# Kernel optimization log

Measured on AMD Instinct MI355X. Metric: run time of the kernel, lower is better.

The kernel has to match this reference:

```python
import jax, jax.numpy as jnp
import numpy as np

N = 50000          # nodes
E = 500000         # edges
EMB = 64           # hidden_size
R = 2              # DDE num_rounds
RR = 2             # DDE num_reverse_rounds
PRED_IN = 4 * EMB + 4 + 4 * (R + RR)  # 276


def setup_inputs() -> dict:
    key = jax.random.key(0)
    ks = jax.random.split(key, 10)
    x = jax.random.normal(ks[0], (N, EMB), jnp.float32)
    edge_index = jax.random.randint(ks[1], (2, E), 0, N, dtype=jnp.int64)
    edge_attr = jax.random.normal(ks[2], (E, EMB), jnp.float32)
    topic_signal = jax.random.uniform(ks[3], (N, 2), dtype=jnp.float32)
    q_emb = jax.random.normal(ks[4], (E, EMB), jnp.float32)
    # learned parameters
    non_text_emb = jax.random.normal(ks[5], (1, EMB), jnp.float32)
    W1 = jax.random.normal(ks[6], (PRED_IN, EMB), jnp.float32) / np.sqrt(PRED_IN)
    b1 = jnp.zeros((EMB,), jnp.float32)
    W2 = jax.random.normal(ks[7], (EMB, 1), jnp.float32) / np.sqrt(EMB)
    b2 = jnp.zeros((1,), jnp.float32)
    return dict(x=x, edge_index=edge_index, edge_attr=edge_attr,
                topic_signal=topic_signal, q_emb=q_emb,
                non_text_emb=non_text_emb, W1=W1, b1=b1, W2=W2, b2=b2)


def _segment_mean(data, seg, num_segments):
    # mean aggregation as in PyG MessagePassing(aggr='mean'); empty segments -> 0
    s = jax.ops.segment_sum(data, seg, num_segments=num_segments)
    cnt = jax.ops.segment_sum(jnp.ones((seg.shape[0],), data.dtype), seg,
                              num_segments=num_segments)
    return s / jnp.maximum(cnt, 1.0)[:, None]


def reference(x, edge_index, edge_attr, topic_signal, q_emb,
              non_text_emb, W1, b1, W2, b2):
    src, dst = edge_index[0], edge_index[1]
    # replace all-zero node rows with the learned non-text entity embedding
    zero_mask = jnp.all(x == 0, axis=1)
    x = jnp.where(zero_mask[:, None], non_text_emb[0], x)

    feats = [x, topic_signal]  # topic_pe = True
    # DDE forward rounds: aggregate src -> dst along edge_index
    h = topic_signal
    for _ in range(R):
        h = _segment_mean(h[src], dst, N)
        feats.append(h)
    # DDE reverse rounds: flipped edges (dst -> src)
    h = topic_signal
    for _ in range(RR):
        h = _segment_mean(h[dst], src, N)
        feats.append(h)

    h_e = jnp.concatenate(feats, axis=1)                      # [N, EMB+2+2*(R+RR)]
    h_triple = jnp.concatenate([q_emb, h_e[src], edge_attr, h_e[dst]], axis=1)  # [E, PRED_IN]
    hidden = jax.nn.relu(h_triple @ W1 + b1)                  # [E, EMB]
    return (hidden @ W2 + b2).squeeze(-1)                     # [E]
```

## Files before the change

### kernel.cpp

```cpp
#include <hip/hip_runtime.h>
#include <cstdint>
#include <cstddef>


typedef __bf16 bf16x8 __attribute__((ext_vector_type(8)));
typedef float f32x4 __attribute__((ext_vector_type(4)));

__device__ __forceinline__ unsigned int f2bf1(float f) {
    unsigned int u = __float_as_uint(f);
    return (u + 0x7fffu + ((u >> 16) & 1u)) >> 16;
}
__device__ __forceinline__ unsigned int pk2(float a, float b) {
    return f2bf1(a) | (f2bf1(b) << 16);
}
__device__ __forceinline__ bf16x8 cvt8v(float4 a, float4 b) {
    bf16x8 r;
    r[0] = (__bf16)a.x; r[1] = (__bf16)a.y; r[2] = (__bf16)a.z; r[3] = (__bf16)a.w;
    r[4] = (__bf16)b.x; r[5] = (__bf16)b.y; r[6] = (__bf16)b.z; r[7] = (__bf16)b.w;
    return r;
}

#define GL16(gp, lp)                                                        \
    __builtin_amdgcn_global_load_lds(                                       \
        (const __attribute__((address_space(1))) void*)(gp),                \
        (__attribute__((address_space(3))) void*)(lp), 16, 0, 0)


__global__ void k_detect(const int* __restrict__ idx, int E, int* __restrict__ flag) {
    int e = blockIdx.x * blockDim.x + threadIdx.x;
    bool nz = (e < E) && (idx[2 * e + 1] != 0);
    unsigned long long m = __ballot(nz);
    if (m != 0ull && (threadIdx.x & 63) == 0) atomicOr(flag, 1);
}

__global__ void k_convert(const int* __restrict__ idx, int E, const int* __restrict__ flag,
                          int* __restrict__ src_i, int* __restrict__ dst_i,
                          int* __restrict__ cnt_dst, int* __restrict__ cnt_src,
                          unsigned short* __restrict__ pos_f, unsigned short* __restrict__ pos_r) {
    int e = blockIdx.x * blockDim.x + threadIdx.x;
    if (e >= E) return;
    int s, d;
    if (*flag) { s = idx[e];     d = idx[E + e]; }
    else       { s = idx[2 * e]; d = idx[2 * E + 2 * e]; }
    src_i[e] = s; dst_i[e] = d;
    pos_f[e] = (unsigned short)atomicAdd(&cnt_dst[d], 1);
    pos_r[e] = (unsigned short)atomicAdd(&cnt_src[s], 1);
}

__global__ void k_scan(const int* __restrict__ cnt_dst, const int* __restrict__ cnt_src,
                       int* __restrict__ off_f, int* __restrict__ off_r, int N) {
    const int* cnt = (blockIdx.x == 0) ? cnt_dst : cnt_src;
    int* off       = (blockIdx.x == 0) ? off_f   : off_r;
    const int t = threadIdx.x;
    const int C = (N + 1023) / 1024;
    int lo = t * C, hi = lo + C; if (hi > N) hi = N; if (lo > N) lo = N;
    int sum = 0;
    for (int i = lo; i < hi; ++i) sum += cnt[i];
    __shared__ int wsum[16];
    int lane = t & 63, wv = t >> 6;
    int v = sum;
    for (int ofs = 1; ofs < 64; ofs <<= 1) {
        int u = __shfl_up(v, ofs);
        if (lane >= ofs) v += u;
    }
    if (lane == 63) wsum[wv] = v;
    __syncthreads();
    if (wv == 0) {
        int x = (lane < 16) ? wsum[lane] : 0;
        for (int ofs = 1; ofs < 16; ofs <<= 1) {
            int u = __shfl_up(x, ofs);
            if (lane >= ofs) x += u;
        }
        if (lane < 16) wsum[lane] = x;
    }
    __syncthreads();
    int base = (wv > 0 ? wsum[wv - 1] : 0) + (v - sum);
    for (int i = lo; i < hi; ++i) { off[i] = base; base += cnt[i]; }
}

__global__ void k_fill(const int* __restrict__ src_i, const int* __restrict__ dst_i,
                       const unsigned short* __restrict__ pos_f, const unsigned short* __restrict__ pos_r,
                       const int* __restrict__ off_f, const int* __restrict__ off_r,
                       int* __restrict__ csr_f, int* __restrict__ csr_r, int E) {
    int e = blockIdx.x * blockDim.x + threadIdx.x;
    if (e >= E) return;
    int s = src_i[e], d = dst_i[e];
    csr_f[off_f[d] + pos_f[e]] = s;
    csr_r[off_r[s] + pos_r[e]] = d;
}

__global__ void k_round(const int* __restrict__ off_f, const int* __restrict__ csr_f,
                        const int* __restrict__ off_r, const int* __restrict__ csr_r,
                        const float* __restrict__ hf_in,
                        const float* __restrict__ hr_in,
                        float* __restrict__ f_out, float* __restrict__ r_out,
                        int N, int E) {
    int gid = blockIdx.x * blockDim.x + threadIdx.x;
    if (gid >= 2 * N) return;
    const bool rev = gid >= N;
    const int n = rev ? gid - N : gid;
    const int* __restrict__ off = rev ? off_r : off_f;
    const int* __restrict__ csr = rev ? csr_r : csr_f;
    const float2* __restrict__ h = (const float2*)(rev ? hr_in : hf_in);
    float2* __restrict__ o = (float2*)(rev ? r_out : f_out);
    int b = off[n], e = (n + 1 < N) ? off[n + 1] : E;
    float sx = 0.f, sy = 0.f;
    for (int j = b; j < e; ++j) { float2 t = h[csr[j]]; sx += t.x; sy += t.y; }
    float inv = 1.0f / (float)max(e - b, 1);
    o[n] = make_float2(sx * inv, sy * inv);
}

__global__ void k_build(const float* __restrict__ x, const float* __restrict__ topic,
                        const float* __restrict__ nte,
                        const float* __restrict__ f1, const float* __restrict__ f2,
                        const float* __restrict__ r1, const float* __restrict__ r2,
                        unsigned short* __restrict__ he, int N) {
    int n = blockIdx.x * blockDim.x + threadIdx.x;
    if (n >= N) return;
    const float4* xr = (const float4*)(x + (size_t)n * 64);
    float4 v[16];
    bool allz = true;
#pragma unroll
    for (int i = 0; i < 16; ++i) {
        v[i] = xr[i];
        allz = allz && (v[i].x == 0.f && v[i].y == 0.f && v[i].z == 0.f && v[i].w == 0.f);
    }
    const float4* nr = (const float4*)nte;
    unsigned int row[40];
#pragma unroll
    for (int i = 0; i < 16; ++i) {
        float4 s = allz ? nr[i] : v[i];
        row[2 * i]     = pk2(s.x, s.y);
        row[2 * i + 1] = pk2(s.z, s.w);
    }
    row[32] = pk2(topic[2 * n], topic[2 * n + 1]);
    row[33] = pk2(f1[2 * n], f1[2 * n + 1]);
    row[34] = pk2(f2[2 * n], f2[2 * n + 1]);
    row[35] = pk2(r1[2 * n], r1[2 * n + 1]);
    row[36] = pk2(r2[2 * n], r2[2 * n + 1]);
    row[37] = 0u; row[38] = 0u; row[39] = 0u;
    uint4* dst = (uint4*)(he + (size_t)n * 80);
#pragma unroll
    for (int i = 0; i < 10; ++i) dst[i] = ((const uint4*)row)[i];
}

__global__ void k_w1t(const float* __restrict__ W1, unsigned short* __restrict__ W1T) {
    int i = blockIdx.x * blockDim.x + threadIdx.x;
    if (i >= 64 * 288) return;
    int col = i / 288, pk = i - col * 288;
    int k = 0; bool valid = true;
    if (pk < 64)       { k = pk; }
    else if (pk < 128) { k = 138 + (pk - 64); }
    else if (pk < 208) { int j = pk - 128; k = 64 + j;  valid = j < 74; }
    else               { int j = pk - 208; k = 202 + j; valid = j < 74; }
    float v = valid ? W1[k * 64 + col] : 0.f;
    W1T[col * 288 + pk] = (unsigned short)f2bf1(v);
}


__launch_bounds__(128, 2)
__global__ void k_gemm(const float* __restrict__ q_emb,
                       const float* __restrict__ edge_attr,
                       const unsigned short* __restrict__ he,
                       const unsigned short* __restrict__ W1Tg,
                       const int* __restrict__ src_i, const int* __restrict__ dst_i,
                       const float* __restrict__ b1, const float* __restrict__ W2,
                       const float* __restrict__ b2, float* __restrict__ out, int E)
{
    __shared__ __align__(64) char smem[57344];
    const int tid = threadIdx.x;
    const int w = tid >> 6, l = tid & 63, c = l & 15, q = l >> 4;
    const int NW = gridDim.x * 2;
    const int gw = blockIdx.x * 2 + w;
    const int ntiles = E / 16;

#pragma unroll
    for (int jj = 0; jj < 18; ++jj) {
        int j = w * 18 + jj;
        GL16((const char*)W1Tg + j * 1024 + l * 16, smem + j * 1024);
    }

    char* buf0 = smem + 36864 + (w * 2) * 5120;
    char* buf1 = buf0 + 5120;

    int T = gw;
    {
        int e0 = T * 16 + (l & 15);
        int s0 = src_i[e0], d0 = dst_i[e0];
#pragma unroll
        for (int j = 0; j < 5; ++j) {
            int ch = j * 4 + (l >> 4);
            int node = ch < 10 ? s0 : d0;
            int chunk = ch < 10 ? ch : ch - 10;
            GL16((const char*)he + (size_t)node * 160 + chunk * 16, buf0 + j * 1024);
        }
    }
    const float* qr0 = q_emb     + (size_t)(T * 16 + c) * 64 + q * 8;
    const float* ar0 = edge_attr + (size_t)(T * 16 + c) * 64 + q * 8;
    float4 qc0 = *(const float4*)qr0,        qc1 = *(const float4*)(qr0 + 4);
    float4 qc2 = *(const float4*)(qr0 + 32), qc3 = *(const float4*)(qr0 + 36);
    float4 ec0 = *(const float4*)ar0,        ec1 = *(const float4*)(ar0 + 4);
    float4 ec2 = *(const float4*)(ar0 + 32), ec3 = *(const float4*)(ar0 + 36);
    int si_n, di_n;
    {
        int en = min(T + NW, ntiles - 1) * 16 + (l & 15);
        si_n = src_i[en]; di_n = dst_i[en];
    }
    float b1v[4], w2v[4];
#pragma unroll
    for (int ct = 0; ct < 4; ++ct) { b1v[ct] = b1[ct * 16 + c]; w2v[ct] = W2[ct * 16 + c]; }
    const float bb = b2[0];
    __syncthreads();

    int cur = 0;
    while (T < ntiles) {
        const int Tn = T + NW;
        const bool more = Tn < ntiles;
        float4 qn0, qn1, qn2, qn3, en0, en1, en2, en3;
        int si_f = si_n, di_f = di_n;
        char* sbuf = cur ? buf0 : buf1;
        char* cbuf = cur ? buf1 : buf0;

        if (more) {
            const float* qr = q_emb     + (size_t)(Tn * 16 + c) * 64 + q * 8;
            const float* ar = edge_attr + (size_t)(Tn * 16 + c) * 64 + q * 8;
            qn0 = *(const float4*)qr;        qn1 = *(const float4*)(qr + 4);
            qn2 = *(const float4*)(qr + 32); qn3 = *(const float4*)(qr + 36);
            en0 = *(const float4*)ar;        en1 = *(const float4*)(ar + 4);
            en2 = *(const float4*)(ar + 32); en3 = *(const float4*)(ar + 36);
#pragma unroll
            for (int j = 0; j < 5; ++j) {
                int ch = j * 4 + (l >> 4);
                int node = ch < 10 ? si_n : di_n;
                int chunk = ch < 10 ? ch : ch - 10;
                GL16((const char*)he + (size_t)node * 160 + chunk * 16, sbuf + j * 1024);
            }
            int ef = min(Tn + NW, ntiles - 1) * 16 + (l & 15);
            si_f = src_i[ef]; di_f = dst_i[ef];
            asm volatile("s_waitcnt vmcnt(15)" ::: "memory");
        } else {
            qn0 = qc0; qn1 = qc1; qn2 = qc2; qn3 = qc3;
            en0 = ec0; en1 = ec1; en2 = ec2; en3 = ec3;
            asm volatile("s_waitcnt vmcnt(0)" ::: "memory");
        }
        __builtin_amdgcn_sched_barrier(0);

        f32x4 acc0 = {}, acc1 = {}, acc2 = {}, acc3 = {};
        const char* wrow = smem + c * 576 + q * 16;
#define BF(ct, ks) (*(const bf16x8*)(wrow + (ct) * 9216 + (ks) * 64))
#define HEF(pl) (*(const bf16x8*)(cbuf + (pl) * 256 + c * 16))
#define KST(ks, A)                                                                 \
        {                                                                          \
            bf16x8 a_ = (A);                                                       \
            acc0 = __builtin_amdgcn_mfma_f32_16x16x32_bf16(a_, BF(0, ks), acc0, 0, 0, 0); \
            acc1 = __builtin_amdgcn_mfma_f32_16x16x32_bf16(a_, BF(1, ks), acc1, 0, 0, 0); \
            acc2 = __builtin_amdgcn_mfma_f32_16x16x32_bf16(a_, BF(2, ks), acc2, 0, 0, 0); \
            acc3 = __builtin_amdgcn_mfma_f32_16x16x32_bf16(a_, BF(3, ks), acc3, 0, 0, 0); \
        }
        KST(0, cvt8v(qc0, qc1))
        KST(1, cvt8v(qc2, qc3))
        KST(2, cvt8v(ec0, ec1))
        KST(3, cvt8v(ec2, ec3))
        KST(4, HEF(q))
        KST(5, HEF(q + 4))
        KST(6, HEF(q + 8))
        KST(7, HEF(q + 12))
        KST(8, HEF(q + 16))
#undef KST
#undef HEF
#undef BF

        float pr[4];
#pragma unroll
        for (int r = 0; r < 4; ++r) {
            float h0 = fmaxf(acc0[r] + b1v[0], 0.f);
            float h1 = fmaxf(acc1[r] + b1v[1], 0.f);
            float h2 = fmaxf(acc2[r] + b1v[2], 0.f);
            float h3 = fmaxf(acc3[r] + b1v[3], 0.f);
            float p = fmaf(h0, w2v[0], fmaf(h1, w2v[1], fmaf(h2, w2v[2], h3 * w2v[3])));
            p += __shfl_xor(p, 1);
            p += __shfl_xor(p, 2);
            p += __shfl_xor(p, 4);
            p += __shfl_xor(p, 8);
            pr[r] = p;
        }
        if (c == 0) {
            *(float4*)&out[T * 16 + q * 4] =
                make_float4(pr[0] + bb, pr[1] + bb, pr[2] + bb, pr[3] + bb);
        }

        qc0 = qn0; qc1 = qn1; qc2 = qn2; qc3 = qn3;
        ec0 = en0; ec1 = en1; ec2 = en2; ec3 = en3;
        si_n = si_f; di_n = di_f;
        T = Tn; cur ^= 1;
    }
}


extern "C" void kernel_launch(void* const* d_in, const int* in_sizes, int n_in,
                              void* d_out, int out_size, void* d_ws, size_t ws_size,
                              hipStream_t stream)
{
    const float* x         = (const float*)d_in[0];
    const int*   eidx      = (const int*)  d_in[1];
    const float* edge_attr = (const float*)d_in[2];
    const float* topic     = (const float*)d_in[3];
    const float* q_emb     = (const float*)d_in[4];
    const float* nte       = (const float*)d_in[5];
    const float* W1        = (const float*)d_in[6];
    const float* b1        = (const float*)d_in[7];
    const float* W2        = (const float*)d_in[8];
    const float* b2        = (const float*)d_in[9];
    float* out = (float*)d_out;

    const int E = out_size;
    const int N = in_sizes[0] / 64;

    char* ws = (char*)d_ws;
    int* flag  = (int*)ws;
    int* src_i = (int*)(ws + 16);
    int* dst_i = src_i + E;
    int* off_f = dst_i + E;
    int* off_r = off_f + N;
    float* fblk = (float*)(off_r + N);
    float* f1 = fblk;
    float* f2 = fblk + 2 * (size_t)N;
    float* r1 = fblk + 4 * (size_t)N;
    float* r2 = fblk + 6 * (size_t)N;
    int* cnt_dst = (int*)f1;
    int* cnt_src = cnt_dst + N;
    char* heblk = (char*)(fblk + 8 * (size_t)N);
    unsigned short* pos_f = (unsigned short*)heblk;
    unsigned short* pos_r = pos_f + E;
    int* csr_f = (int*)(pos_r + E);
    int* csr_r = csr_f + E;
    unsigned short* he = (unsigned short*)heblk;
    size_t he_bytes = (size_t)N * 160;
    size_t trans_bytes = (size_t)E * 12;
    size_t heblk_bytes = he_bytes > trans_bytes ? he_bytes : trans_bytes;
    unsigned short* W1T = (unsigned short*)(heblk + heblk_bytes);

    size_t needed = 16 + (size_t)8 * E + (size_t)8 * N + (size_t)32 * N + heblk_bytes + 64 * 288 * 2;
    if (ws_size < needed) return;

    hipMemsetAsync(flag, 0, 16, stream);
    hipMemsetAsync(cnt_dst, 0, (size_t)8 * N, stream);

    const int gE = (E + 255) / 256;
    const int gN = (N + 255) / 256;
    const int gN2 = (2 * N + 255) / 256;

    k_detect <<<gE, 256, 0, stream>>>(eidx, E, flag);
    k_convert<<<gE, 256, 0, stream>>>(eidx, E, flag, src_i, dst_i,
                                      cnt_dst, cnt_src, pos_f, pos_r);
    k_scan   <<<2, 1024, 0, stream>>>(cnt_dst, cnt_src, off_f, off_r, N);
    k_fill   <<<gE, 256, 0, stream>>>(src_i, dst_i, pos_f, pos_r, off_f, off_r,
                                      csr_f, csr_r, E);
    k_round  <<<gN2, 256, 0, stream>>>(off_f, csr_f, off_r, csr_r, topic, topic, f1, r1, N, E);
    k_round  <<<gN2, 256, 0, stream>>>(off_f, csr_f, off_r, csr_r, f1, r1, f2, r2, N, E);
    k_build  <<<gN, 256, 0, stream>>>(x, topic, nte, f1, f2, r1, r2, he, N);
    k_w1t    <<<(64 * 288 + 255) / 256, 256, 0, stream>>>(W1, W1T);

    k_gemm<<<512, 128, 0, stream>>>(q_emb, edge_attr, he, W1T,
                                    src_i, dst_i, b1, W2, b2, out, E);
}
```

Measured before the change: 559.1 us.

## Use fragment-ordered W1T layout, 4 waves per block, deeper index prefetch

Reorders the transposed bf16 W1 into MFMA fragment order so each lane's B-operand LDS read is contiguous (l*16 stride), which should remove bank conflicts from the old 576-byte row stride. Raises the GEMM block to 4 waves sharing one LDS copy of the weights, halving the weight staging per wave and doubling waves per CU. It also prefetches src/dst indices two tiles ahead to hide gather-address latency. The cost is larger LDS per block (77.8KB), which may limit blocks per CU, and more register pressure.

```diff
diff --git a/kernel.cpp b/kernel.cpp
--- a/kernel.cpp
+++ b/kernel.cpp
@@ -147,18 +147,23 @@
 __global__ void k_w1t(const float* __restrict__ W1, unsigned short* __restrict__ W1T) {
     int i = blockIdx.x * blockDim.x + threadIdx.x;
     if (i >= 64 * 288) return;
-    int col = i / 288, pk = i - col * 288;
+    int j = i & 7;
+    int l = (i >> 3) & 63;
+    int t36 = i >> 9;
+    int ks = t36 % 9, ct = t36 / 9;
+    int col = ct * 16 + (l & 15);
+    int pk = ks * 32 + (l >> 4) * 8 + j;
     int k = 0; bool valid = true;
     if (pk < 64)       { k = pk; }
     else if (pk < 128) { k = 138 + (pk - 64); }
-    else if (pk < 208) { int j = pk - 128; k = 64 + j;  valid = j < 74; }
-    else               { int j = pk - 208; k = 202 + j; valid = j < 74; }
+    else if (pk < 208) { int jj = pk - 128; k = 64 + jj;  valid = jj < 74; }
+    else               { int jj = pk - 208; k = 202 + jj; valid = jj < 74; }
     float v = valid ? W1[k * 64 + col] : 0.f;
-    W1T[col * 288 + pk] = (unsigned short)f2bf1(v);
-}
-
-
-__launch_bounds__(128, 2)
+    W1T[i] = (unsigned short)f2bf1(v);
+}
+
+
+__launch_bounds__(256, 2)
 __global__ void k_gemm(const float* __restrict__ q_emb,
                        const float* __restrict__ edge_attr,
                        const unsigned short* __restrict__ he,
@@ -167,29 +172,29 @@
                        const float* __restrict__ b1, const float* __restrict__ W2,
                        const float* __restrict__ b2, float* __restrict__ out, int E)
 {
-    __shared__ __align__(64) char smem[57344];
+    __shared__ __align__(64) char smem[77824];
     const int tid = threadIdx.x;
     const int w = tid >> 6, l = tid & 63, c = l & 15, q = l >> 4;
-    const int NW = gridDim.x * 2;
-    const int gw = blockIdx.x * 2 + w;
+    const int NW = gridDim.x * 4;
+    const int gw = blockIdx.x * 4 + w;
     const int ntiles = E / 16;
 
 #pragma unroll
-    for (int jj = 0; jj < 18; ++jj) {
-        int j = w * 18 + jj;
+    for (int jj = 0; jj < 9; ++jj) {
+        int j = w * 9 + jj;
         GL16((const char*)W1Tg + j * 1024 + l * 16, smem + j * 1024);
     }
 
-    char* buf0 = smem + 36864 + (w * 2) * 5120;
+    char* buf0 = smem + 36864 + w * 10240;
     char* buf1 = buf0 + 5120;
 
     int T = gw;
     {
-        int e0 = T * 16 + (l & 15);
+        int e0 = T * 16 + c;
         int s0 = src_i[e0], d0 = dst_i[e0];
 #pragma unroll
         for (int j = 0; j < 5; ++j) {
-            int ch = j * 4 + (l >> 4);
+            int ch = j * 4 + q;
             int node = ch < 10 ? s0 : d0;
             int chunk = ch < 10 ? ch : ch - 10;
             GL16((const char*)he + (size_t)node * 160 + chunk * 16, buf0 + j * 1024);
@@ -201,10 +206,12 @@
     float4 qc2 = *(const float4*)(qr0 + 32), qc3 = *(const float4*)(qr0 + 36);
     float4 ec0 = *(const float4*)ar0,        ec1 = *(const float4*)(ar0 + 4);
     float4 ec2 = *(const float4*)(ar0 + 32), ec3 = *(const float4*)(ar0 + 36);
-    int si_n, di_n;
+    int siA, diA, siB, diB;
     {
-        int en = min(T + NW, ntiles - 1) * 16 + (l & 15);
-        si_n = src_i[en]; di_n = dst_i[en];
+        int eA = min(T + NW, ntiles - 1) * 16 + c;
+        int eB = min(T + 2 * NW, ntiles - 1) * 16 + c;
+        siA = src_i[eA]; diA = dst_i[eA];
+        siB = src_i[eB]; diB = dst_i[eB];
     }
     float b1v[4], w2v[4];
 #pragma unroll
@@ -217,7 +224,7 @@
         const int Tn = T + NW;
         const bool more = Tn < ntiles;
         float4 qn0, qn1, qn2, qn3, en0, en1, en2, en3;
-        int si_f = si_n, di_f = di_n;
+        int siC = siB, diC = diB;
         char* sbuf = cur ? buf0 : buf1;
         char* cbuf = cur ? buf1 : buf0;
 
@@ -230,13 +237,13 @@
             en2 = *(const float4*)(ar + 32); en3 = *(const float4*)(ar + 36);
 #pragma unroll
             for (int j = 0; j < 5; ++j) {
-                int ch = j * 4 + (l >> 4);
-                int node = ch < 10 ? si_n : di_n;
+                int ch = j * 4 + q;
+                int node = ch < 10 ? siA : diA;
                 int chunk = ch < 10 ? ch : ch - 10;
                 GL16((const char*)he + (size_t)node * 160 + chunk * 16, sbuf + j * 1024);
             }
-            int ef = min(Tn + NW, ntiles - 1) * 16 + (l & 15);
-            si_f = src_i[ef]; di_f = dst_i[ef];
+            int eC = min(T + 3 * NW, ntiles - 1) * 16 + c;
+            siC = src_i[eC]; diC = dst_i[eC];
             asm volatile("s_waitcnt vmcnt(15)" ::: "memory");
         } else {
             qn0 = qc0; qn1 = qc1; qn2 = qc2; qn3 = qc3;
@@ -246,8 +253,8 @@
         __builtin_amdgcn_sched_barrier(0);
 
         f32x4 acc0 = {}, acc1 = {}, acc2 = {}, acc3 = {};
-        const char* wrow = smem + c * 576 + q * 16;
-#define BF(ct, ks) (*(const bf16x8*)(wrow + (ct) * 9216 + (ks) * 64))
+        const char* wbase = smem + (size_t)l * 16;
+#define BF(ct, ks) (*(const bf16x8*)(wbase + (ct) * 9216 + (ks) * 1024))
 #define HEF(pl) (*(const bf16x8*)(cbuf + (pl) * 256 + c * 16))
 #define KST(ks, A)                                                                 \
         {                                                                          \
@@ -291,7 +298,7 @@
 
         qc0 = qn0; qc1 = qn1; qc2 = qn2; qc3 = qn3;
         ec0 = en0; ec1 = en1; ec2 = en2; ec3 = en3;
-        si_n = si_f; di_n = di_f;
+        siA = siB; diA = diB; siB = siC; diB = diC;
         T = Tn; cur ^= 1;
     }
 }
@@ -361,6 +368,6 @@
     k_build  <<<gN, 256, 0, stream>>>(x, topic, nte, f1, f2, r1, r2, he, N);
     k_w1t    <<<(64 * 288 + 255) / 256, 256, 0, stream>>>(W1, W1T);
 
-    k_gemm<<<512, 128, 0, stream>>>(q_emb, edge_attr, he, W1T,
+    k_gemm<<<512, 256, 0, stream>>>(q_emb, edge_attr, he, W1T,
                                     src_i, dst_i, b1, W2, b2, out, E);
 }
```

Result: no change. 554.8 us (-0.8%).
